# Kernel optimization log

Measured on AMD Instinct MI355X. Metric: run time of the kernel, lower is better.

## Reference

```python
import jax, jax.numpy as jnp
import numpy as np

NUM_ITERATIONS = 3


def squash(t, axis=-1):
    # scale = |t|^2 / (1 + |t|^2); out = scale * t / |t|  (matches torch source exactly)
    norm = jnp.sum(t * t, axis=axis, keepdims=True)
    scale = norm / (1.0 + norm)
    return scale * t / jnp.sqrt(norm)


def setup_inputs() -> dict:
    key = jax.random.key(0)
    k_u, k_w = jax.random.split(key)
    B, K, R, M, P = 1024, 2, 2336, 4, 16
    u = jax.random.normal(k_u, (B, R, M), dtype=jnp.float32)
    W = jax.random.normal(k_w, (K, R, M, P), dtype=jnp.float32)
    return {"u": u, "W": W}


def reference(u, W):
    # u: [B, R, M]; W: [K, R, M, P]
    # torch: matmul(u[:,None,:,None,:], W) -> [B,K,R,1,P]; we drop the singleton dim.
    u_ji = jnp.einsum('brm,krmp->bkrp', u, W)  # [B, K, R, P]
    b = jnp.zeros_like(u_ji)
    v = None
    for i in range(NUM_ITERATIONS):
        c = jax.nn.softmax(b, axis=2)                      # softmax over routes
        v = squash(jnp.sum(c * u_ji, axis=2, keepdims=True))  # [B, K, 1, P]
        if i != NUM_ITERATIONS - 1:
            b = b + jnp.sum(u_ji * v, axis=-1, keepdims=True)  # agreement, broadcasts over P
    v = jnp.squeeze(v, axis=2)                 # [B, K, P]
    classes = jnp.sqrt(jnp.sum(v * v, axis=-1))  # [B, K]
    return classes
```

## Files before the change

### kernel.cpp

```cpp
#include <hip/hip_runtime.h>
#include <hip/hip_fp16.h>
#include <math.h>


#define THREADS 512
#define NWAVE 8
#define RR 2336
#define KK 2

#if __has_builtin(__builtin_amdgcn_fdot2)
typedef _Float16 h2v __attribute__((ext_vector_type(2)));
static __device__ __forceinline__ float dot2h(__half2 a, __half2 b, float c) {
    h2v av, bv;
    __builtin_memcpy(&av, &a, 4);
    __builtin_memcpy(&bv, &b, 4);
    return __builtin_amdgcn_fdot2(av, bv, c, false);
}
#else
static __device__ __forceinline__ float dot2h(__half2 a, __half2 b, float c) {
    float2 fa = __half22float2(a), fb = __half22float2(b);
    return fmaf(fa.x, fb.x, fmaf(fa.y, fb.y, c));
}
#endif

__global__ __launch_bounds__(256)
void w_repack_kernel(const float* __restrict__ W, __half2* __restrict__ Wt)
{
    const int n = KK * RR * 8;
    for (int j = blockIdx.x * 256 + threadIdx.x; j < n; j += gridDim.x * 256) {
        const int p2 = j & 7;
        const int rk = j >> 3;
        const float* wp = W + (size_t)rk * 64;
        const float x0 = wp[0*16 + 2*p2],     x1 = wp[1*16 + 2*p2];
        const float x2 = wp[2*16 + 2*p2],     x3 = wp[3*16 + 2*p2];
        const float y0 = wp[0*16 + 2*p2 + 1], y1 = wp[1*16 + 2*p2 + 1];
        const float y2 = wp[2*16 + 2*p2 + 1], y3 = wp[3*16 + 2*p2 + 1];
        __half2* o = Wt + (size_t)j * 4;
        o[0] = __floats2half2_rn(x0, x1);
        o[1] = __floats2half2_rn(x2, x3);
        o[2] = __floats2half2_rn(y0, y1);
        o[3] = __floats2half2_rn(y2, y3);
    }
}

__global__ __launch_bounds__(THREADS, 2)
void caps_routing_kernel(const float* __restrict__ u,
                         const __half2* __restrict__ Wt,
                         float* __restrict__ out)
{
    __shared__ __half uji[RR * 16];
    __shared__ float  red[2][NWAVE][17];

    const int bi   = blockIdx.x;
    const int b    = bi >> 1;
    const int k    = bi & 1;
    const int tid  = threadIdx.x;
    const int lane = tid & 63;
    const int wave = tid >> 6;
    const int p2   = lane & 7;
    const int g    = lane >> 3;

    const float4* __restrict__ u4p = (const float4*)u;
    const float4* __restrict__ w4t = (const float4*)Wt + (size_t)k * RR * 8 + p2;

    float sA = 0.0f, sB = 0.0f;
    {
        const int rbase = wave * 8 + g;
        float4 uu_n = u4p[b * RR + rbase];
        float4 wv_n = w4t[(size_t)rbase * 8];
        #pragma unroll 4
        for (int i = 0; i < 37; ++i) {
            const float4 uu = uu_n;
            const float4 wv = wv_n;
            const int r = i * 64 + rbase;
            if (i + 1 < 37) {
                int rn = (i + 1) * 64 + rbase;
                rn = (rn < RR) ? rn : (RR - 1);
                uu_n = u4p[b * RR + rn];
                wv_n = w4t[(size_t)rn * 8];
            }
            const __half2 u01 = __floats2half2_rn(uu.x, uu.y);
            const __half2 u23 = __floats2half2_rn(uu.z, uu.w);
            const __half2* hm = (const __half2*)&wv;
            const float ax = dot2h(u01, hm[0], dot2h(u23, hm[1], 0.0f));
            const float ay = dot2h(u01, hm[2], dot2h(u23, hm[3], 0.0f));
            if (r < RR) {
                sA += ax; sB += ay;
                *(__half2*)(uji + r * 16 + p2 * 2) = __floats2half2_rn(ax, ay);
            }
        }
    }
    sA += __shfl_xor(sA, 8);  sB += __shfl_xor(sB, 8);
    sA += __shfl_xor(sA, 16); sB += __shfl_xor(sB, 16);
    sA += __shfl_xor(sA, 32); sB += __shfl_xor(sB, 32);
    if (lane < 8) {
        red[0][wave][2 * p2]     = sA;
        red[0][wave][2 * p2 + 1] = sB;
    }
    __syncthreads();

    float vcum[8];

    {
        float col = 0.0f;
        if (lane < 16) {
            #pragma unroll
            for (int w = 0; w < NWAVE; ++w) col += red[0][w][lane];
        }
        float nr = col * col;
        nr += __shfl_xor(nr, 1);
        nr += __shfl_xor(nr, 2);
        nr += __shfl_xor(nr, 4);
        nr += __shfl_xor(nr, 8);
        const float inv  = 1.0f / (float)RR;
        const float norm = nr * inv * inv;
        const float f    = sqrtf(norm) / (1.0f + norm);
        const float vnew = col * inv * f;
        #pragma unroll
        for (int i = 0; i < 8; ++i) vcum[i] = __shfl(vnew, (lane & 1) * 8 + i);
    }

    #pragma unroll 1
    for (int it = 1; it < 3; ++it) {
        const int buf = it & 1;

        __half2 v2[4];
        #pragma unroll
        for (int i = 0; i < 4; ++i) v2[i] = __floats2half2_rn(vcum[2*i], vcum[2*i+1]);

        float4 raw[10];
        #pragma unroll
        for (int s = 0; s < 10; ++s) {
            int row = s * 256 + wave * 32 + (lane >> 1);
            row = (row < RR) ? row : (RR - 1);
            raw[s] = *(const float4*)((const char*)uji + row * 32 + (lane & 1) * 16);
        }

        float s8[8] = {0,0,0,0,0,0,0,0};
        float se = 0.0f;
        #pragma unroll
        for (int s = 0; s < 10; ++s) {
            const bool ok = (s * 256 + wave * 32 + (lane >> 1)) < RR;
            const __half2* hp = (const __half2*)&raw[s];
            float d = dot2h(hp[0], v2[0],
                      dot2h(hp[1], v2[1],
                      dot2h(hp[2], v2[2],
                      dot2h(hp[3], v2[3], 0.0f))));
            d += __shfl_xor(d, 1);
            float e = ok ? __expf(d) : 0.0f;
            se += e;
            #pragma unroll
            for (int q = 0; q < 4; ++q) {
                float2 f = __half22float2(hp[q]);
                s8[2*q]   = fmaf(f.x, e, s8[2*q]);
                s8[2*q+1] = fmaf(f.y, e, s8[2*q+1]);
            }
        }

        #pragma unroll
        for (int o = 2; o <= 32; o <<= 1) {
            se += __shfl_xor(se, o);
            #pragma unroll
            for (int i = 0; i < 8; ++i) s8[i] += __shfl_xor(s8[i], o);
        }
        if (lane < 2) {
            #pragma unroll
            for (int i = 0; i < 8; ++i) red[buf][wave][(lane & 1) * 8 + i] = s8[i];
            if (lane == 0) red[buf][wave][16] = se;
        }
        __syncthreads();

        {
            float col = 0.0f;
            if (lane < 17) {
                #pragma unroll
                for (int w = 0; w < NWAVE; ++w) col += red[buf][w][lane];
            }
            float nr = col * col;
            nr += __shfl_xor(nr, 1);
            nr += __shfl_xor(nr, 2);
            nr += __shfl_xor(nr, 4);
            nr += __shfl_xor(nr, 8);
            const float se_t = __shfl(col, 16);
            const float inv  = 1.0f / se_t;
            const float norm = nr * inv * inv;
            if (it == 1) {
                const float f    = sqrtf(norm) / (1.0f + norm);
                const float vnew = col * inv * f;
                #pragma unroll
                for (int i = 0; i < 8; ++i) vcum[i] += __shfl(vnew, (lane & 1) * 8 + i);
            } else if (wave == 0 && lane == 0) {
                out[b * KK + k] = norm / (1.0f + norm);
            }
        }
    }
}

extern "C" void kernel_launch(void* const* d_in, const int* in_sizes, int n_in,
                              void* d_out, int out_size, void* d_ws, size_t ws_size,
                              hipStream_t stream) {
    const float* u = (const float*)d_in[0];
    const float* W = (const float*)d_in[1];
    float* out = (float*)d_out;
    __half2* Wt = (__half2*)d_ws;

    w_repack_kernel<<<dim3(256), dim3(256), 0, stream>>>(W, Wt);
    caps_routing_kernel<<<dim3(2048), dim3(THREADS), 0, stream>>>(u, Wt, out);
}
```

Baseline: 140.9 us.

## Keep per-route predictions in registers instead of shared memory

After: 173.3 us. 1.23x slower.

```diff
diff --git a/kernel.cpp b/kernel.cpp
--- a/kernel.cpp
+++ b/kernel.cpp
@@ -26,20 +26,19 @@
 __global__ __launch_bounds__(256)
 void w_repack_kernel(const float* __restrict__ W, __half2* __restrict__ Wt)
 {
-    const int n = KK * RR * 8;
+    const int n = KK * 8 * RR;
     for (int j = blockIdx.x * 256 + threadIdx.x; j < n; j += gridDim.x * 256) {
-        const int p2 = j & 7;
-        const int rk = j >> 3;
-        const float* wp = W + (size_t)rk * 64;
-        const float x0 = wp[0*16 + 2*p2],     x1 = wp[1*16 + 2*p2];
-        const float x2 = wp[2*16 + 2*p2],     x3 = wp[3*16 + 2*p2];
-        const float y0 = wp[0*16 + 2*p2 + 1], y1 = wp[1*16 + 2*p2 + 1];
-        const float y2 = wp[2*16 + 2*p2 + 1], y3 = wp[3*16 + 2*p2 + 1];
+        const int r  = j % RR;
+        const int kq = j / RR;
+        const int q  = kq & 7;
+        const int k  = kq >> 3;
+        const float* wp = W + (size_t)(k * RR + r) * 64;
+        const int p0 = 2 * q, p1 = 2 * q + 1;
         __half2* o = Wt + (size_t)j * 4;
-        o[0] = __floats2half2_rn(x0, x1);
-        o[1] = __floats2half2_rn(x2, x3);
-        o[2] = __floats2half2_rn(y0, y1);
-        o[3] = __floats2half2_rn(y2, y3);
+        o[0] = __floats2half2_rn(wp[0*16 + p0], wp[1*16 + p0]);
+        o[1] = __floats2half2_rn(wp[2*16 + p0], wp[3*16 + p0]);
+        o[2] = __floats2half2_rn(wp[0*16 + p1], wp[1*16 + p1]);
+        o[3] = __floats2half2_rn(wp[2*16 + p1], wp[3*16 + p1]);
     }
 }
 
@@ -48,8 +47,7 @@
                          const __half2* __restrict__ Wt,
                          float* __restrict__ out)
 {
-    __shared__ __half uji[RR * 16];
-    __shared__ float  red[2][NWAVE][17];
+    __shared__ float red[2][NWAVE][17];
 
     const int bi   = blockIdx.x;
     const int b    = bi >> 1;
@@ -57,116 +55,84 @@
     const int tid  = threadIdx.x;
     const int lane = tid & 63;
     const int wave = tid >> 6;
-    const int p2   = lane & 7;
-    const int g    = lane >> 3;
 
     const float4* __restrict__ u4p = (const float4*)u;
-    const float4* __restrict__ w4t = (const float4*)Wt + (size_t)k * RR * 8 + p2;
+    const float4* __restrict__ wqp = (const float4*)Wt + (size_t)k * 8 * RR;
 
-    float sA = 0.0f, sB = 0.0f;
-    {
-        const int rbase = wave * 8 + g;
-        float4 uu_n = u4p[b * RR + rbase];
-        float4 wv_n = w4t[(size_t)rbase * 8];
-        #pragma unroll 4
-        for (int i = 0; i < 37; ++i) {
-            const float4 uu = uu_n;
-            const float4 wv = wv_n;
-            const int r = i * 64 + rbase;
-            if (i + 1 < 37) {
-                int rn = (i + 1) * 64 + rbase;
-                rn = (rn < RR) ? rn : (RR - 1);
-                uu_n = u4p[b * RR + rn];
-                wv_n = w4t[(size_t)rn * 8];
-            }
-            const __half2 u01 = __floats2half2_rn(uu.x, uu.y);
-            const __half2 u23 = __floats2half2_rn(uu.z, uu.w);
+    const bool ok4 = tid < (RR - 4 * THREADS);
+
+    __half2 uji[5][8];
+    #pragma unroll
+    for (int j = 0; j < 5; ++j) {
+        const int r  = tid + j * THREADS;
+        const int rc = (r < RR) ? r : (RR - 1);
+        const bool ok = (j < 4) | ok4;
+        const float4 uu = u4p[b * RR + rc];
+        const __half2 u01 = __floats2half2_rn(uu.x, uu.y);
+        const __half2 u23 = __floats2half2_rn(uu.z, uu.w);
+        #pragma unroll
+        for (int q = 0; q < 8; ++q) {
+            const float4 wv = wqp[(size_t)q * RR + rc];
             const __half2* hm = (const __half2*)&wv;
-            const float ax = dot2h(u01, hm[0], dot2h(u23, hm[1], 0.0f));
-            const float ay = dot2h(u01, hm[2], dot2h(u23, hm[3], 0.0f));
-            if (r < RR) {
-                sA += ax; sB += ay;
-                *(__half2*)(uji + r * 16 + p2 * 2) = __floats2half2_rn(ax, ay);
-            }
+            float ax = dot2h(u01, hm[0], dot2h(u23, hm[1], 0.0f));
+            float ay = dot2h(u01, hm[2], dot2h(u23, hm[3], 0.0f));
+            ax = ok ? ax : 0.0f;
+            ay = ok ? ay : 0.0f;
+            uji[j][q] = __floats2half2_rn(ax, ay);
         }
     }
-    sA += __shfl_xor(sA, 8);  sB += __shfl_xor(sB, 8);
-    sA += __shfl_xor(sA, 16); sB += __shfl_xor(sB, 16);
-    sA += __shfl_xor(sA, 32); sB += __shfl_xor(sB, 32);
-    if (lane < 8) {
-        red[0][wave][2 * p2]     = sA;
-        red[0][wave][2 * p2 + 1] = sB;
-    }
-    __syncthreads();
 
-    float vcum[8];
-
-    {
-        float col = 0.0f;
-        if (lane < 16) {
-            #pragma unroll
-            for (int w = 0; w < NWAVE; ++w) col += red[0][w][lane];
-        }
-        float nr = col * col;
-        nr += __shfl_xor(nr, 1);
-        nr += __shfl_xor(nr, 2);
-        nr += __shfl_xor(nr, 4);
-        nr += __shfl_xor(nr, 8);
-        const float inv  = 1.0f / (float)RR;
-        const float norm = nr * inv * inv;
-        const float f    = sqrtf(norm) / (1.0f + norm);
-        const float vnew = col * inv * f;
-        #pragma unroll
-        for (int i = 0; i < 8; ++i) vcum[i] = __shfl(vnew, (lane & 1) * 8 + i);
-    }
+    float vcum_l = 0.0f;
 
     #pragma unroll 1
-    for (int it = 1; it < 3; ++it) {
-        const int buf = it & 1;
-
-        __half2 v2[4];
+    for (int it = 0; it < 3; ++it) {
+        __half2 v2[8];
         #pragma unroll
-        for (int i = 0; i < 4; ++i) v2[i] = __floats2half2_rn(vcum[2*i], vcum[2*i+1]);
-
-        float4 raw[10];
-        #pragma unroll
-        for (int s = 0; s < 10; ++s) {
-            int row = s * 256 + wave * 32 + (lane >> 1);
-            row = (row < RR) ? row : (RR - 1);
-            raw[s] = *(const float4*)((const char*)uji + row * 32 + (lane & 1) * 16);
+        for (int q = 0; q < 8; ++q) {
+            const float va = __shfl(vcum_l, 2 * q);
+            const float vb = __shfl(vcum_l, 2 * q + 1);
+            v2[q] = __floats2half2_rn(va, vb);
         }
 
-        float s8[8] = {0,0,0,0,0,0,0,0};
+        float t16[16] = {0,0,0,0,0,0,0,0,0,0,0,0,0,0,0,0};
         float se = 0.0f;
         #pragma unroll
-        for (int s = 0; s < 10; ++s) {
-            const bool ok = (s * 256 + wave * 32 + (lane >> 1)) < RR;
-            const __half2* hp = (const __half2*)&raw[s];
-            float d = dot2h(hp[0], v2[0],
-                      dot2h(hp[1], v2[1],
-                      dot2h(hp[2], v2[2],
-                      dot2h(hp[3], v2[3], 0.0f))));
-            d += __shfl_xor(d, 1);
-            float e = ok ? __expf(d) : 0.0f;
+        for (int j = 0; j < 5; ++j) {
+            const bool ok = (j < 4) | ok4;
+            float e;
+            if (it == 0) {
+                e = ok ? 1.0f : 0.0f;
+            } else {
+                const float d = dot2h(uji[j][0], v2[0],
+                                dot2h(uji[j][1], v2[1],
+                                dot2h(uji[j][2], v2[2],
+                                dot2h(uji[j][3], v2[3],
+                                dot2h(uji[j][4], v2[4],
+                                dot2h(uji[j][5], v2[5],
+                                dot2h(uji[j][6], v2[6],
+                                dot2h(uji[j][7], v2[7], 0.0f))))))));
+                e = ok ? __expf(d) : 0.0f;
+            }
             se += e;
             #pragma unroll
-            for (int q = 0; q < 4; ++q) {
-                float2 f = __half22float2(hp[q]);
-                s8[2*q]   = fmaf(f.x, e, s8[2*q]);
-                s8[2*q+1] = fmaf(f.y, e, s8[2*q+1]);
+            for (int q = 0; q < 8; ++q) {
+                const float2 h = __half22float2(uji[j][q]);
+                t16[2*q]   = fmaf(h.x, e, t16[2*q]);
+                t16[2*q+1] = fmaf(h.y, e, t16[2*q+1]);
             }
         }
 
         #pragma unroll
-        for (int o = 2; o <= 32; o <<= 1) {
+        for (int o = 1; o <= 32; o <<= 1) {
             se += __shfl_xor(se, o);
             #pragma unroll
-            for (int i = 0; i < 8; ++i) s8[i] += __shfl_xor(s8[i], o);
+            for (int p = 0; p < 16; ++p) t16[p] += __shfl_xor(t16[p], o);
         }
-        if (lane < 2) {
+        const int buf = it & 1;
+        if (lane == 0) {
             #pragma unroll
-            for (int i = 0; i < 8; ++i) red[buf][wave][(lane & 1) * 8 + i] = s8[i];
-            if (lane == 0) red[buf][wave][16] = se;
+            for (int p = 0; p < 16; ++p) red[buf][wave][p] = t16[p];
+            red[buf][wave][16] = se;
         }
         __syncthreads();
 
@@ -184,11 +150,10 @@
             const float se_t = __shfl(col, 16);
             const float inv  = 1.0f / se_t;
             const float norm = nr * inv * inv;
-            if (it == 1) {
+            if (it < 2) {
                 const float f    = sqrtf(norm) / (1.0f + norm);
                 const float vnew = col * inv * f;
-                #pragma unroll
-                for (int i = 0; i < 8; ++i) vcum[i] += __shfl(vnew, (lane & 1) * 8 + i);
+                if (lane < 16) vcum_l += vnew;
             } else if (wave == 0 && lane == 0) {
                 out[b * KK + k] = norm / (1.0f + norm);
             }
```
